# Kernel optimization log

Hardware: AMD Instinct MI355X
Metric: run time of the kernel (lower is better)

Reference implementation:

```python
import jax, jax.numpy as jnp
import numpy as np
from jax import lax

B, T, H, IN = 2048, 2048, 25, 1


def setup_inputs() -> dict:
    key = jax.random.key(0)
    ks = jax.random.split(key, 7)
    s = 1.0 / np.sqrt(H)  # PyTorch LSTM init scale
    return {
        "x": jax.random.normal(ks[0], (B, T, IN), dtype=jnp.float32),
        "w_ih": jax.random.uniform(ks[1], (4 * H, IN), jnp.float32, -s, s),
        "w_hh": jax.random.uniform(ks[2], (4 * H, H), jnp.float32, -s, s),
        "b_ih": jax.random.uniform(ks[3], (4 * H,), jnp.float32, -s, s),
        "b_hh": jax.random.uniform(ks[4], (4 * H,), jnp.float32, -s, s),
        "w_dense": jax.random.uniform(ks[5], (1, H), jnp.float32, -s, s),
        "b_dense": jax.random.uniform(ks[6], (1,), jnp.float32, -s, s),
    }


def reference(x, w_ih, w_hh, b_ih, b_hh, w_dense, b_dense):
    # x: [B, T, 1] -> scan over time on [T, B, *]
    xt = jnp.swapaxes(x, 0, 1)                     # [T, B, IN]
    x_proj = xt @ w_ih.T + (b_ih + b_hh)           # [T, B, 4H], input projection precomputed

    def step(carry, xp):
        h, c = carry
        gates = xp + h @ w_hh.T                    # [B, 4H]
        i, f, g, o = jnp.split(gates, 4, axis=-1)  # PyTorch gate order i,f,g,o
        i = jax.nn.sigmoid(i)
        f = jax.nn.sigmoid(f)
        g = jnp.tanh(g)
        o = jax.nn.sigmoid(o)
        c = f * c + i * g
        h = o * jnp.tanh(c)
        return (h, c), h

    h0 = jnp.zeros((x.shape[0], H), dtype=x.dtype)
    c0 = jnp.zeros((x.shape[0], H), dtype=x.dtype)
    _, hs = lax.scan(step, (h0, c0), x_proj)       # hs: [T, B, H]
    hs = jnp.swapaxes(hs, 0, 1)                    # [B, T, H]
    return hs @ w_dense.T + b_dense                # [B, T, 1]
```

## Files before the change

### kernel.cpp

```cpp
#include <hip/hip_runtime.h>

#define T_LEN 2048
#define HID   25
#define LOG2E 1.4426950408889634f

typedef float vf4 __attribute__((vector_size(16), may_alias));
typedef float f2  __attribute__((ext_vector_type(2)));

__device__ __forceinline__ float fast_rcp(float x) { return __builtin_amdgcn_rcpf(x); }
__device__ __forceinline__ float fast_exp2(float x) { return __builtin_amdgcn_exp2f(x); }


__global__ __attribute__((amdgpu_flat_work_group_size(256, 256),
                          amdgpu_waves_per_eu(2, 2)))
void lstm_fused(
    const float* __restrict__ x,
    const float* __restrict__ w_ih,
    const float* __restrict__ w_hh,
    const float* __restrict__ b_ih,
    const float* __restrict__ b_hh,
    const float* __restrict__ w_dense,
    const float* __restrict__ b_dense,
    float* __restrict__ out)
{
    const int tid = threadIdx.x;
    const int l   = tid & 63;
    const int u   = l & 31;
    const int hh  = l >> 5;
    const int w   = tid >> 6;
    const int b   = blockIdx.x * 4 + w;
    const bool act = u < HID;

    __shared__ __align__(16) float hbuf[4][64];
    __shared__ float hist[4][64][65];

    const float si = -LOG2E, sg = 2.f * LOG2E;

    const int   rowA = hh ? (HID + u)     : u;
    const int   rowB = hh ? (3 * HID + u) : (2 * HID + u);
    const float scB  = hh ? si : sg;

    f2 wA2[12], wB2[12];
#pragma unroll
    for (int m = 0; m < 12; ++m) {
        wA2[m] = act ? f2{si  * w_hh[rowA * HID + m], si  * w_hh[rowA * HID + m + 12]} : f2{0.f, 0.f};
        wB2[m] = act ? f2{scB * w_hh[rowB * HID + m], scB * w_hh[rowB * HID + m + 12]} : f2{0.f, 0.f};
    }
    const float wA24 = act ? si  * w_hh[rowA * HID + 24] : 0.f;
    const float wB24 = act ? scB * w_hh[rowB * HID + 24] : 0.f;
    const float bA   = act ? si  * (b_ih[rowA] + b_hh[rowA]) : 0.f;
    const float bB   = act ? scB * (b_ih[rowB] + b_hh[rowB]) : 0.f;
    const float wxA  = act ? si  * w_ih[rowA] : 0.f;
    const float wxB  = act ? scB * w_ih[rowB] : 0.f;
    const float bd   = b_dense[0];

    float wdv[HID];
#pragma unroll
    for (int i = 0; i < HID; ++i) wdv[i] = w_dense[i];

    hbuf[w][l] = 0.f;

    const int slot = hh ? ((u < 12) ? 2 * u : (u < 24) ? 2 * u - 23 : u)
                        : (l + 32);
    float* hwr = &hbuf[w][slot];
    const vf4* r4 = (const vf4*)&hbuf[w][0];
    const float* hbF = &hbuf[w][0];

    const int hcol = hh ? u : (32 + l);

    const float4* __restrict__ xp = (const float4*)(x + (size_t)b * T_LEN);
    float* __restrict__ orow = out + (size_t)b * T_LEN;

    f2 hp[12];
#pragma unroll
    for (int m = 0; m < 12; ++m) hp[m] = f2{0.f, 0.f};
    float h24 = 0.f;

    float c = 0.f;
    float4 xcur = xp[0];

    for (int it = 0; it < T_LEN / 4; ++it) {
        const int nx = (it + 1 < T_LEN / 4) ? it + 1 : it;
        float4 xnext = xp[nx];
        float xs[4] = {xcur.x, xcur.y, xcur.z, xcur.w};

#pragma unroll
        for (int s = 0; s < 4; ++s) {
            const float xv = xs[s];
            const int t = 4 * it + s;

            f2 accA = f2{fmaf(xv, wxA, bA), 0.f};
            f2 accB = f2{fmaf(xv, wxB, bB), 0.f};
#pragma unroll
            for (int m = 0; m < 12; ++m) {
                const f2 h = hp[m];
                accA = __builtin_elementwise_fma(h, wA2[m], accA);
                accB = __builtin_elementwise_fma(h, wB2[m], accB);
            }
            const float aA = accA.x + fmaf(h24, wA24, accA.y);
            const float aB = accB.x + fmaf(h24, wB24, accB.y);

            const float rA = fast_rcp(1.f + fast_exp2(aA));
            const float rB = fast_rcp(1.f + fast_exp2(aB));
            const float tB = fmaf(-2.f, rB, 1.f);

            const float p  = rA * tB;
            const float pX = __shfl_xor(p, 32, 64);

            c = fmaf(rA, c, pX);
            const float tC = fmaf(-2.f, fast_rcp(1.f + fast_exp2(2.f * LOG2E * c)), 1.f);
            const float hn = rB * tC;

            *hwr = hn;
            hist[w][t & 63][hcol] = hn;
            __asm__ __volatile__("" ::: "memory");
            {
                vf4 a0 = r4[0], a1 = r4[1], a2 = r4[2];
                vf4 a3 = r4[3], a4 = r4[4], a5 = r4[5];
                hp[0]  = f2{a0[0], a0[1]}; hp[1]  = f2{a0[2], a0[3]};
                hp[2]  = f2{a1[0], a1[1]}; hp[3]  = f2{a1[2], a1[3]};
                hp[4]  = f2{a2[0], a2[1]}; hp[5]  = f2{a2[2], a2[3]};
                hp[6]  = f2{a3[0], a3[1]}; hp[7]  = f2{a3[2], a3[3]};
                hp[8]  = f2{a4[0], a4[1]}; hp[9]  = f2{a4[2], a4[3]};
                hp[10] = f2{a5[0], a5[1]}; hp[11] = f2{a5[2], a5[3]};
                h24 = hbF[24];
            }
            __asm__ __volatile__("" ::: "memory");

            if ((t & 63) == 63) {
                const float* hrow = &hist[w][l][0];
                float ys = 0.f;
#pragma unroll
                for (int i = 0; i < HID; ++i)
                    ys = fmaf(hrow[i], wdv[i], ys);
                orow[(t & ~63) + l] = ys + bd;
            }
        }
        xcur = xnext;
    }
}

extern "C" void kernel_launch(void* const* d_in, const int* in_sizes, int n_in,
                              void* d_out, int out_size, void* d_ws, size_t ws_size,
                              hipStream_t stream) {
    const float* x       = (const float*)d_in[0];
    const float* w_ih    = (const float*)d_in[1];
    const float* w_hh    = (const float*)d_in[2];
    const float* b_ih    = (const float*)d_in[3];
    const float* b_hh    = (const float*)d_in[4];
    const float* w_dense = (const float*)d_in[5];
    const float* b_dense = (const float*)d_in[6];
    float* out = (float*)d_out;

    lstm_fused<<<dim3(512), dim3(256), 0, stream>>>(x, w_ih, w_hh, b_ih, b_hh,
                                                    w_dense, b_dense, out);
}
```

Before: 587.6 us.

## Interleave two independent batch sequences per wavefront to hide recurrence latency

Each wavefront now carries two batch rows and alternates their LSTM steps, so one sequence's dependent chain of math, shuffle and LDS round-trips can overlap the other's. Grid size is halved and waves_per_eu drops to 1 so the doubled register state fits. The goal is instruction-level parallelism inside a wave instead of relying on multiple resident waves, at the cost of doubled LDS per block and fewer blocks in flight.

New measurement: 754.4 us. 1.28x slower.

```diff
diff --git a/kernel.cpp b/kernel.cpp
--- a/kernel.cpp
+++ b/kernel.cpp
@@ -12,7 +12,7 @@
 
 
 __global__ __attribute__((amdgpu_flat_work_group_size(256, 256),
-                          amdgpu_waves_per_eu(2, 2)))
+                          amdgpu_waves_per_eu(1, 1)))
 void lstm_fused(
     const float* __restrict__ x,
     const float* __restrict__ w_ih,
@@ -28,11 +28,11 @@
     const int u   = l & 31;
     const int hh  = l >> 5;
     const int w   = tid >> 6;
-    const int b   = blockIdx.x * 4 + w;
+    const int cb0 = (blockIdx.x * 4 + w) * 2;
     const bool act = u < HID;
 
-    __shared__ __align__(16) float hbuf[4][64];
-    __shared__ float hist[4][64][65];
+    __shared__ __align__(16) float hbuf[4][2][64];
+    __shared__ float hist[4][2][64][65];
 
     const float si = -LOG2E, sg = 2.f * LOG2E;
 
@@ -58,85 +58,100 @@
 #pragma unroll
     for (int i = 0; i < HID; ++i) wdv[i] = w_dense[i];
 
-    hbuf[w][l] = 0.f;
+    hbuf[w][0][l] = 0.f;
+    hbuf[w][1][l] = 0.f;
 
     const int slot = hh ? ((u < 12) ? 2 * u : (u < 24) ? 2 * u - 23 : u)
                         : (l + 32);
-    float* hwr = &hbuf[w][slot];
-    const vf4* r4 = (const vf4*)&hbuf[w][0];
-    const float* hbF = &hbuf[w][0];
-
     const int hcol = hh ? u : (32 + l);
 
-    const float4* __restrict__ xp = (const float4*)(x + (size_t)b * T_LEN);
-    float* __restrict__ orow = out + (size_t)b * T_LEN;
+    float* hwrA = &hbuf[w][0][slot];
+    float* hwrB = &hbuf[w][1][slot];
+    const vf4* r4A = (const vf4*)&hbuf[w][0][0];
+    const vf4* r4B = (const vf4*)&hbuf[w][1][0];
+    const float* hbFA = &hbuf[w][0][0];
+    const float* hbFB = &hbuf[w][1][0];
+    float (*histA)[65] = hist[w][0];
+    float (*histB)[65] = hist[w][1];
 
-    f2 hp[12];
+    const float4* __restrict__ xpA = (const float4*)(x + (size_t)cb0 * T_LEN);
+    const float4* __restrict__ xpB = (const float4*)(x + (size_t)(cb0 + 1) * T_LEN);
+    float* __restrict__ orowA = out + (size_t)cb0 * T_LEN;
+    float* __restrict__ orowB = out + (size_t)(cb0 + 1) * T_LEN;
+
+    f2 hpA[12], hpB[12];
 #pragma unroll
-    for (int m = 0; m < 12; ++m) hp[m] = f2{0.f, 0.f};
-    float h24 = 0.f;
+    for (int m = 0; m < 12; ++m) { hpA[m] = f2{0.f, 0.f}; hpB[m] = f2{0.f, 0.f}; }
+    float h24A = 0.f, h24B = 0.f;
+    float cA = 0.f, cB = 0.f;
 
-    float c = 0.f;
-    float4 xcur = xp[0];
+    float4 xcurA = xpA[0], xcurB = xpB[0];
+
+    auto step = [&](f2* hp, float& h24, float& c, float xv, int t,
+                    float* hwr, const vf4* r4, const float* hbF,
+                    float (*histc)[65], float* __restrict__ orow) {
+        f2 accA = f2{fmaf(xv, wxA, bA), 0.f};
+        f2 accB = f2{fmaf(xv, wxB, bB), 0.f};
+#pragma unroll
+        for (int m = 0; m < 12; ++m) {
+            const f2 h = hp[m];
+            accA = __builtin_elementwise_fma(h, wA2[m], accA);
+            accB = __builtin_elementwise_fma(h, wB2[m], accB);
+        }
+        const float aA = accA.x + fmaf(h24, wA24, accA.y);
+        const float aB = accB.x + fmaf(h24, wB24, accB.y);
+
+        const float rA = fast_rcp(1.f + fast_exp2(aA));
+        const float rB = fast_rcp(1.f + fast_exp2(aB));
+        const float tB = fmaf(-2.f, rB, 1.f);
+
+        const float p  = rA * tB;
+        const float pX = __shfl_xor(p, 32, 64);
+
+        c = fmaf(rA, c, pX);
+        const float tC = fmaf(-2.f, fast_rcp(1.f + fast_exp2(2.f * LOG2E * c)), 1.f);
+        const float hn = rB * tC;
+
+        *hwr = hn;
+        histc[t & 63][hcol] = hn;
+        __asm__ __volatile__("" ::: "memory");
+        {
+            vf4 a0 = r4[0], a1 = r4[1], a2 = r4[2];
+            vf4 a3 = r4[3], a4 = r4[4], a5 = r4[5];
+            hp[0]  = f2{a0[0], a0[1]}; hp[1]  = f2{a0[2], a0[3]};
+            hp[2]  = f2{a1[0], a1[1]}; hp[3]  = f2{a1[2], a1[3]};
+            hp[4]  = f2{a2[0], a2[1]}; hp[5]  = f2{a2[2], a2[3]};
+            hp[6]  = f2{a3[0], a3[1]}; hp[7]  = f2{a3[2], a3[3]};
+            hp[8]  = f2{a4[0], a4[1]}; hp[9]  = f2{a4[2], a4[3]};
+            hp[10] = f2{a5[0], a5[1]}; hp[11] = f2{a5[2], a5[3]};
+            h24 = hbF[24];
+        }
+        __asm__ __volatile__("" ::: "memory");
+
+        if ((t & 63) == 63) {
+            const float* hrow = &histc[l][0];
+            float ys = 0.f;
+#pragma unroll
+            for (int i = 0; i < HID; ++i)
+                ys = fmaf(hrow[i], wdv[i], ys);
+            orow[(t & ~63) + l] = ys + bd;
+        }
+    };
 
     for (int it = 0; it < T_LEN / 4; ++it) {
         const int nx = (it + 1 < T_LEN / 4) ? it + 1 : it;
-        float4 xnext = xp[nx];
-        float xs[4] = {xcur.x, xcur.y, xcur.z, xcur.w};
+        float4 xnA = xpA[nx], xnB = xpB[nx];
+        float xsA[4] = {xcurA.x, xcurA.y, xcurA.z, xcurA.w};
+        float xsB[4] = {xcurB.x, xcurB.y, xcurB.z, xcurB.w};
 
 #pragma unroll
         for (int s = 0; s < 4; ++s) {
-            const float xv = xs[s];
             const int t = 4 * it + s;
-
-            f2 accA = f2{fmaf(xv, wxA, bA), 0.f};
-            f2 accB = f2{fmaf(xv, wxB, bB), 0.f};
-#pragma unroll
-            for (int m = 0; m < 12; ++m) {
-                const f2 h = hp[m];
-                accA = __builtin_elementwise_fma(h, wA2[m], accA);
-                accB = __builtin_elementwise_fma(h, wB2[m], accB);
-            }
-            const float aA = accA.x + fmaf(h24, wA24, accA.y);
-            const float aB = accB.x + fmaf(h24, wB24, accB.y);
-
-            const float rA = fast_rcp(1.f + fast_exp2(aA));
-            const float rB = fast_rcp(1.f + fast_exp2(aB));
-            const float tB = fmaf(-2.f, rB, 1.f);
-
-            const float p  = rA * tB;
-            const float pX = __shfl_xor(p, 32, 64);
-
-            c = fmaf(rA, c, pX);
-            const float tC = fmaf(-2.f, fast_rcp(1.f + fast_exp2(2.f * LOG2E * c)), 1.f);
-            const float hn = rB * tC;
-
-            *hwr = hn;
-            hist[w][t & 63][hcol] = hn;
-            __asm__ __volatile__("" ::: "memory");
-            {
-                vf4 a0 = r4[0], a1 = r4[1], a2 = r4[2];
-                vf4 a3 = r4[3], a4 = r4[4], a5 = r4[5];
-                hp[0]  = f2{a0[0], a0[1]}; hp[1]  = f2{a0[2], a0[3]};
-                hp[2]  = f2{a1[0], a1[1]}; hp[3]  = f2{a1[2], a1[3]};
-                hp[4]  = f2{a2[0], a2[1]}; hp[5]  = f2{a2[2], a2[3]};
-                hp[6]  = f2{a3[0], a3[1]}; hp[7]  = f2{a3[2], a3[3]};
-                hp[8]  = f2{a4[0], a4[1]}; hp[9]  = f2{a4[2], a4[3]};
-                hp[10] = f2{a5[0], a5[1]}; hp[11] = f2{a5[2], a5[3]};
-                h24 = hbF[24];
-            }
-            __asm__ __volatile__("" ::: "memory");
-
-            if ((t & 63) == 63) {
-                const float* hrow = &hist[w][l][0];
-                float ys = 0.f;
-#pragma unroll
-                for (int i = 0; i < HID; ++i)
-                    ys = fmaf(hrow[i], wdv[i], ys);
-                orow[(t & ~63) + l] = ys + bd;
-            }
+            step(hpA, h24A, cA, xsA[s], t, hwrA, r4A, hbFA, histA, orowA);
+            step(hpB, h24B, cB, xsB[s], t, hwrB, r4B, hbFB, histB, orowB);
         }
-        xcur = xnext;
+        xcurA = xnA;
+        xcurB = xnB;
     }
 }
 
@@ -152,6 +167,6 @@
     const float* b_dense = (const float*)d_in[6];
     float* out = (float*)d_out;
 
-    lstm_fused<<<dim3(512), dim3(256), 0, stream>>>(x, w_ih, w_hh, b_ih, b_hh,
+    lstm_fused<<<dim3(256), dim3(256), 0, stream>>>(x, w_ih, w_hh, b_ih, b_hh,
                                                     w_dense, b_dense, out);
 }
```
